# Optimization experiments

Hardware: AMD Instinct MI355X
Metric: run time of the kernel (lower is better)

## Reference

```python
import jax, jax.numpy as jnp
import numpy as np

B, N, IN_DIM, OUT_DIM, H = 4, 2048, 1024, 1024, 16
HEAD_DIM = OUT_DIM // H  # 64


def setup_inputs() -> dict:
    key = jax.random.key(0)
    k_x, k_q, k_k, k_v, k_o = jax.random.split(key, 5)
    s = 1.0 / np.sqrt(IN_DIM)
    return {
        "x": jax.random.normal(k_x, (B, N, IN_DIM), dtype=jnp.float32),
        "w_q": jax.random.normal(k_q, (IN_DIM, OUT_DIM), dtype=jnp.float32) * s,
        "w_k": jax.random.normal(k_k, (IN_DIM, OUT_DIM), dtype=jnp.float32) * s,
        "w_v": jax.random.normal(k_v, (IN_DIM, OUT_DIM), dtype=jnp.float32) * s,
        "w_out": jax.random.normal(k_o, (OUT_DIM, OUT_DIM), dtype=jnp.float32) * s,
    }


def reference(x, w_q, w_k, w_v, w_out):
    b, n, _ = x.shape
    scale = 1.0 / jnp.sqrt(jnp.float32(HEAD_DIM))
    # QKV projections, split into heads: [b, h, n, d]
    q = (x @ w_q).reshape(b, n, H, HEAD_DIM).transpose(0, 2, 1, 3)
    k = (x @ w_k).reshape(b, n, H, HEAD_DIM).transpose(0, 2, 1, 3)
    v = (x @ w_v).reshape(b, n, H, HEAD_DIM).transpose(0, 2, 1, 3)
    # full score matrix [b, h, q, k]
    scores = jnp.einsum("bhqd,bhkd->bhqk", q, k) * scale
    # NOTE: source applies softmax over dim=1 (the HEAD axis) — reproduce exactly
    attn = jax.nn.softmax(scores, axis=1)
    # dropout p=0.0 -> identity
    ctx = jnp.einsum("bhqk,bhkd->bqhd", attn, v).reshape(b, n, OUT_DIM)
    return ctx @ w_out
```

## Files before the change

kernel.cpp:

```cpp
#include <hip/hip_runtime.h>
#include <hip/hip_bf16.h>

typedef unsigned short u16;
typedef unsigned int u32;
typedef __attribute__((ext_vector_type(8))) short short8;
typedef __attribute__((ext_vector_type(4))) float float4v;
typedef __attribute__((ext_vector_type(4))) unsigned int uint4v;
typedef __attribute__((ext_vector_type(2))) unsigned int uint2v;

__device__ __forceinline__ u16 f2bf(float f) {
    union { float f; unsigned int u; } v; v.f = f;
    unsigned int r = v.u + 0x7fffu + ((v.u >> 16) & 1u);
    return (u16)(r >> 16);
}

__device__ __forceinline__ u32 cvtpk(float lo, float hi) {
    u32 r;
    asm("v_cvt_pk_bf16_f32 %0, %1, %2" : "=v"(r) : "v"(lo), "v"(hi));
    return r;
}
__device__ __forceinline__ float bflo(u32 u) {
    union { u32 u; float f; } v; v.u = u << 16; return v.f;
}
__device__ __forceinline__ float bfhi(u32 u) {
    union { u32 u; float f; } v; v.u = u & 0xffff0000u; return v.f;
}

__device__ __forceinline__ void gld_lds16(const u16* g, u16* l) {
    __builtin_amdgcn_global_load_lds(
        (const __attribute__((address_space(1))) u32*)g,
        (__attribute__((address_space(3))) u32*)l, 16, 0, 0);
}

__global__ __launch_bounds__(256) void convert_x(
    const float* __restrict__ x, u16* __restrict__ xb) {
    int i = (blockIdx.x * 256 + threadIdx.x) * 8;
    float4v a = *(const float4v*)&x[i];
    float4v b = *(const float4v*)&x[i + 4];
    u16 tmp[8] __attribute__((aligned(16)));
#pragma unroll
    for (int j = 0; j < 4; ++j) { tmp[j] = f2bf(a[j]); tmp[4 + j] = f2bf(b[j]); }
    *(uint4v*)&xb[i] = *(uint4v*)tmp;
}

__global__ __launch_bounds__(256) void transpose_w(
    const float* __restrict__ w0, const float* __restrict__ w1,
    const float* __restrict__ w2, const float* __restrict__ w3,
    u16* __restrict__ o0, u16* __restrict__ o1,
    u16* __restrict__ o2, u16* __restrict__ o3) {
    __shared__ u16 t[32][33];
    int z = blockIdx.z;
    const float* w = (z == 0) ? w0 : (z == 1) ? w1 : (z == 2) ? w2 : w3;
    u16* o         = (z == 0) ? o0 : (z == 1) ? o1 : (z == 2) ? o2 : o3;
    int bx = blockIdx.x * 32;
    int by = blockIdx.y * 32;
    int x = threadIdx.x, y = threadIdx.y;
#pragma unroll
    for (int i = 0; i < 4; ++i)
        t[y + i * 8][x] = f2bf(w[(size_t)(by + y + i * 8) * 1024 + bx + x]);
    __syncthreads();
#pragma unroll
    for (int i = 0; i < 4; ++i)
        o[(size_t)(bx + y + i * 8) * 1024 + by + x] = t[x][y + i * 8];
}

__global__ __launch_bounds__(256) void gemm_bt(
    const u16* __restrict__ A, const u16* __restrict__ Bt,
    void* __restrict__ Cout, int M, int N, int K, int mode, float oscale) {
    __shared__ __attribute__((aligned(16))) u16 As[128 * 32];
    __shared__ __attribute__((aligned(16))) u16 Bs[128 * 32];
    const int tid = threadIdx.x;
    const int m0 = blockIdx.y * 128;
    const int n0 = blockIdx.x * 128;
    const int wid = tid >> 6;
    const int lane = tid & 63;
    const int ln = lane & 15, kq = lane >> 4;
    const int wm = (wid >> 1) * 64, wn = (wid & 1) * 64;

    float4v acc[4][4] = {};
    for (int k0 = 0; k0 < K; k0 += 32) {
#pragma unroll
        for (int i = 0; i < 2; ++i) {
            int chunk = tid + i * 256;
            int row = chunk >> 2, cg = chunk & 3;
            u16* lA = &As[(size_t)(i * 256 + wid * 64) * 8];
            u16* lB = &Bs[(size_t)(i * 256 + wid * 64) * 8];
            gld_lds16(&A[(size_t)(m0 + row) * K + k0 + cg * 8], lA);
            gld_lds16(&Bt[(size_t)(n0 + row) * K + k0 + cg * 8], lB);
        }
        __syncthreads();
        short8 af[4], bfr[4];
#pragma unroll
        for (int mt = 0; mt < 4; ++mt)
            af[mt] = *(const short8*)&As[(wm + mt * 16 + ln) * 32 + kq * 8];
#pragma unroll
        for (int nt = 0; nt < 4; ++nt)
            bfr[nt] = *(const short8*)&Bs[(wn + nt * 16 + ln) * 32 + kq * 8];
#pragma unroll
        for (int mt = 0; mt < 4; ++mt)
#pragma unroll
            for (int nt = 0; nt < 4; ++nt)
                acc[mt][nt] = __builtin_amdgcn_mfma_f32_16x16x32_bf16(
                    af[mt], bfr[nt], acc[mt][nt], 0, 0, 0);
        __syncthreads();
    }
    if (mode == 0) {
        u16* C = (u16*)Cout;
#pragma unroll
        for (int mt = 0; mt < 4; ++mt)
#pragma unroll
            for (int nt = 0; nt < 4; ++nt)
#pragma unroll
                for (int r = 0; r < 4; ++r) {
                    int row = m0 + wm + mt * 16 + kq * 4 + r;
                    int col = n0 + wn + nt * 16 + ln;
                    C[(size_t)row * N + col] = f2bf(acc[mt][nt][r] * oscale);
                }
    } else if (mode == 1) {
        u16* C = (u16*)Cout;
#pragma unroll
        for (int mt = 0; mt < 4; ++mt)
#pragma unroll
            for (int nt = 0; nt < 4; ++nt)
#pragma unroll
                for (int r = 0; r < 4; ++r) {
                    int t = m0 + wm + mt * 16 + kq * 4 + r;
                    int col = n0 + wn + nt * 16 + ln;
                    int b = t >> 11, n = t & 2047;
                    C[((size_t)(b * 1024 + col)) * 2048 + n] = f2bf(acc[mt][nt][r]);
                }
    } else {
        float* C = (float*)Cout;
#pragma unroll
        for (int mt = 0; mt < 4; ++mt)
#pragma unroll
            for (int nt = 0; nt < 4; ++nt)
#pragma unroll
                for (int r = 0; r < 4; ++r) {
                    int row = m0 + wm + mt * 16 + kq * 4 + r;
                    int col = n0 + wn + nt * 16 + ln;
                    C[(size_t)row * N + col] = acc[mt][nt][r];
                }
    }
}

__global__ __launch_bounds__(1024, 4) void attn_kernel(
    const u16* qb, const u16* __restrict__ kb,
    const u16* __restrict__ vt, u16* cb) {
    __shared__ __attribute__((aligned(16))) u16   Ebuf[3][512 * 36];
    __shared__ __attribute__((aligned(16))) float Dibuf[2][32 * 36];

    const int b = blockIdx.y;
    const int q0 = blockIdx.x * 32;
    const int tid = threadIdx.x;
    const int wid = tid >> 6, lane = tid & 63;
    const int ln = lane & 15, kq = lane >> 4;
    const int h = wid;

    short8 aq[2][2];
#pragma unroll
    for (int mt = 0; mt < 2; ++mt)
#pragma unroll
        for (int kc = 0; kc < 2; ++kc)
            aq[mt][kc] = *(const short8*)&qb[
                (size_t)(b * 2048 + q0 + mt * 16 + ln) * 1024 +
                h * 64 + kc * 32 + kq * 8];

    float4v cacc[2][4] = {};
    short8 bvA[4], bvB[4];

    const int NT = 64;
#pragma unroll 1
    for (int i = 0; i < NT + 2; ++i) {
        short8 bk[2][2];
        if (i < NT) {
            const int kt = i * 32;
#pragma unroll
            for (int kc = 0; kc < 2; ++kc)
#pragma unroll
                for (int nt = 0; nt < 2; ++nt)
                    bk[kc][nt] = *(const short8*)&kb[
                        (size_t)(b * 2048 + kt + nt * 16 + ln) * 1024 +
                        h * 64 + kc * 32 + kq * 8];
        }
        if (i >= 1 && i <= NT) {
            const int kt = (i - 1) * 32;
#pragma unroll
            for (int nt = 0; nt < 4; ++nt)
                bvB[nt] = *(const short8*)&vt[
                    (size_t)(b * 1024 + h * 64 + nt * 16 + ln) * 2048 + kt + kq * 8];
        }
        if (i >= 2) {
            const u16*   Ee = Ebuf[(i - 2) % 3];
            const float* Dd = Dibuf[(i - 2) & 1];
            short8 ap[2];
#pragma unroll
            for (int mt = 0; mt < 2; ++mt) {
                const u16* ep = &Ee[(h * 32 + mt * 16 + ln) * 36 + kq * 8];
                uint2v ea = *(const uint2v*)&ep[0];
                uint2v eb = *(const uint2v*)&ep[4];
                const float* dp = &Dd[(mt * 16 + ln) * 36 + kq * 8];
                float4v g0 = *(const float4v*)&dp[0];
                float4v g1 = *(const float4v*)&dp[4];
                u32 pk[4] __attribute__((aligned(16)));
                pk[0] = cvtpk(bflo(ea[0]) * g0[0], bfhi(ea[0]) * g0[1]);
                pk[1] = cvtpk(bflo(ea[1]) * g0[2], bfhi(ea[1]) * g0[3]);
                pk[2] = cvtpk(bflo(eb[0]) * g1[0], bfhi(eb[0]) * g1[1]);
                pk[3] = cvtpk(bflo(eb[1]) * g1[2], bfhi(eb[1]) * g1[3]);
                ap[mt] = *(short8*)pk;
            }
#pragma unroll
            for (int nt = 0; nt < 4; ++nt)
#pragma unroll
                for (int mt = 0; mt < 2; ++mt)
                    cacc[mt][nt] = __builtin_amdgcn_mfma_f32_16x16x32_bf16(
                        ap[mt], bvA[nt], cacc[mt][nt], 0, 0, 0);
        }
        if (i < NT) {
            float4v sacc[2][2] = {};
#pragma unroll
            for (int kc = 0; kc < 2; ++kc)
#pragma unroll
                for (int mt = 0; mt < 2; ++mt)
#pragma unroll
                    for (int nt = 0; nt < 2; ++nt)
                        sacc[mt][nt] = __builtin_amdgcn_mfma_f32_16x16x32_bf16(
                            bk[kc][nt], aq[mt][kc], sacc[mt][nt], 0, 0, 0);
            u16* Ew = Ebuf[i % 3];
#pragma unroll
            for (int mt = 0; mt < 2; ++mt)
#pragma unroll
                for (int nt = 0; nt < 2; ++nt) {
                    float e0 = exp2f(fminf(sacc[mt][nt][0], 115.0f));
                    float e1 = exp2f(fminf(sacc[mt][nt][1], 115.0f));
                    float e2 = exp2f(fminf(sacc[mt][nt][2], 115.0f));
                    float e3 = exp2f(fminf(sacc[mt][nt][3], 115.0f));
                    uint2v w; w[0] = cvtpk(e0, e1); w[1] = cvtpk(e2, e3);
                    *(uint2v*)&Ew[(h * 32 + mt * 16 + ln) * 36 + nt * 16 + kq * 4] = w;
                }
        }
        if (i >= 1 && i <= NT && tid < 256) {
            const u16* Ee = Ebuf[(i - 1) % 3];
            const int q = tid >> 3, k4 = tid & 7;
            float d0 = 0.f, d1 = 0.f, d2 = 0.f, d3 = 0.f;
#pragma unroll
            for (int hh = 0; hh < 16; ++hh) {
                uint2v e = *(const uint2v*)&Ee[(hh * 32 + q) * 36 + k4 * 4];
                d0 += bflo(e[0]); d1 += bfhi(e[0]);
                d2 += bflo(e[1]); d3 += bfhi(e[1]);
            }
            float4v dv;
            dv[0] = __builtin_amdgcn_rcpf(d0);
            dv[1] = __builtin_amdgcn_rcpf(d1);
            dv[2] = __builtin_amdgcn_rcpf(d2);
            dv[3] = __builtin_amdgcn_rcpf(d3);
            *(float4v*)&Dibuf[(i - 1) & 1][q * 36 + k4 * 4] = dv;
        }
        __syncthreads();
#pragma unroll
        for (int nt = 0; nt < 4; ++nt) bvA[nt] = bvB[nt];
    }

#pragma unroll
    for (int mt = 0; mt < 2; ++mt)
#pragma unroll
        for (int nt = 0; nt < 4; ++nt)
#pragma unroll
            for (int r = 0; r < 4; ++r) {
                int row = b * 2048 + q0 + mt * 16 + kq * 4 + r;
                int col = h * 64 + nt * 16 + ln;
                cb[(size_t)row * 1024 + col] = f2bf(cacc[mt][nt][r]);
            }
}

extern "C" void kernel_launch(void* const* d_in, const int* in_sizes, int n_in,
                              void* d_out, int out_size, void* d_ws, size_t ws_size,
                              hipStream_t stream) {
    const float* x   = (const float*)d_in[0];
    const float* w_q = (const float*)d_in[1];
    const float* w_k = (const float*)d_in[2];
    const float* w_v = (const float*)d_in[3];
    const float* w_o = (const float*)d_in[4];

    char* ws = (char*)d_ws;
    const size_t SZ_W   = (size_t)1024 * 1024 * 2;
    const size_t SZ_TOK = (size_t)8192 * 1024 * 2;
    u16* x_bf  = (u16*)(ws);
    u16* wtq   = (u16*)(ws + SZ_TOK);
    u16* wtk   = (u16*)(ws + SZ_TOK + SZ_W);
    u16* wtv   = (u16*)(ws + SZ_TOK + 2 * SZ_W);
    u16* wto   = (u16*)(ws + SZ_TOK + 3 * SZ_W);
    u16* q_buf = (u16*)(ws + SZ_TOK + 4 * SZ_W);
    u16* k_buf  = (u16*)d_out;
    u16* vt_buf = (u16*)d_out + (size_t)8192 * 1024;

    convert_x<<<4096, 256, 0, stream>>>(x, x_bf);

    transpose_w<<<dim3(32, 32, 4), dim3(32, 8), 0, stream>>>(
        w_q, w_k, w_v, w_o, wtq, wtk, wtv, wto);

    gemm_bt<<<dim3(8, 64), 256, 0, stream>>>(x_bf, wtq, q_buf, 8192, 1024, 1024, 0, 0.18033688f);
    gemm_bt<<<dim3(8, 64), 256, 0, stream>>>(x_bf, wtk, k_buf, 8192, 1024, 1024, 0, 1.0f);
    gemm_bt<<<dim3(8, 64), 256, 0, stream>>>(x_bf, wtv, vt_buf, 8192, 1024, 1024, 1, 1.0f);

    attn_kernel<<<dim3(64, 4), 1024, 0, stream>>>(q_buf, k_buf, vt_buf, q_buf);

    gemm_bt<<<dim3(8, 64), 256, 0, stream>>>(q_buf, wto, d_out, 8192, 1024, 1024, 2, 1.0f);
}
```

Measured before the change: 536.5 us.

## Replace three-stage attention pipeline with 64-key tiles and two barriers per tile

```diff
diff --git a/kernel.cpp b/kernel.cpp
--- a/kernel.cpp
+++ b/kernel.cpp
@@ -7,6 +7,7 @@
 typedef __attribute__((ext_vector_type(4))) float float4v;
 typedef __attribute__((ext_vector_type(4))) unsigned int uint4v;
 typedef __attribute__((ext_vector_type(2))) unsigned int uint2v;
+typedef __attribute__((ext_vector_type(2))) float float2v;
 
 __device__ __forceinline__ u16 f2bf(float f) {
     union { float f; unsigned int u; } v; v.f = f;
@@ -144,11 +145,11 @@
     }
 }
 
-__global__ __launch_bounds__(1024, 4) void attn_kernel(
+__global__ __launch_bounds__(1024) void attn_kernel(
     const u16* qb, const u16* __restrict__ kb,
     const u16* __restrict__ vt, u16* cb) {
-    __shared__ __attribute__((aligned(16))) u16   Ebuf[3][512 * 36];
-    __shared__ __attribute__((aligned(16))) float Dibuf[2][32 * 36];
+    __shared__ __attribute__((aligned(16))) u16   Ebuf[2][512 * 72];
+    __shared__ __attribute__((aligned(16))) float Di[32 * 68];
 
     const int b = blockIdx.y;
     const int q0 = blockIdx.x * 32;
@@ -167,39 +168,83 @@
                 h * 64 + kc * 32 + kq * 8];
 
     float4v cacc[2][4] = {};
-    short8 bvA[4], bvB[4];
-
-    const int NT = 64;
+
 #pragma unroll 1
-    for (int i = 0; i < NT + 2; ++i) {
-        short8 bk[2][2];
-        if (i < NT) {
-            const int kt = i * 32;
+    for (int t = 0; t < 32; ++t) {
+        const int kt = t << 6;
+        u16* E = Ebuf[t & 1];
+
+#pragma unroll
+        for (int c = 0; c < 2; ++c) {
+            short8 bk[2][2];
 #pragma unroll
             for (int kc = 0; kc < 2; ++kc)
 #pragma unroll
                 for (int nt = 0; nt < 2; ++nt)
                     bk[kc][nt] = *(const short8*)&kb[
-                        (size_t)(b * 2048 + kt + nt * 16 + ln) * 1024 +
+                        (size_t)(b * 2048 + kt + c * 32 + nt * 16 + ln) * 1024 +
                         h * 64 + kc * 32 + kq * 8];
+            float4v sacc[2][2] = {};
+#pragma unroll
+            for (int kc = 0; kc < 2; ++kc)
+#pragma unroll
+                for (int mt = 0; mt < 2; ++mt)
+#pragma unroll
+                    for (int nt = 0; nt < 2; ++nt)
+                        sacc[mt][nt] = __builtin_amdgcn_mfma_f32_16x16x32_bf16(
+                            bk[kc][nt], aq[mt][kc], sacc[mt][nt], 0, 0, 0);
+#pragma unroll
+            for (int mt = 0; mt < 2; ++mt)
+#pragma unroll
+                for (int nt = 0; nt < 2; ++nt) {
+                    float e0 = exp2f(fminf(sacc[mt][nt][0], 115.0f));
+                    float e1 = exp2f(fminf(sacc[mt][nt][1], 115.0f));
+                    float e2 = exp2f(fminf(sacc[mt][nt][2], 115.0f));
+                    float e3 = exp2f(fminf(sacc[mt][nt][3], 115.0f));
+                    uint2v w; w[0] = cvtpk(e0, e1); w[1] = cvtpk(e2, e3);
+                    *(uint2v*)&E[(h * 32 + mt * 16 + ln) * 72 +
+                                 c * 32 + nt * 16 + kq * 4] = w;
+                }
         }
-        if (i >= 1 && i <= NT) {
-            const int kt = (i - 1) * 32;
-#pragma unroll
-            for (int nt = 0; nt < 4; ++nt)
-                bvB[nt] = *(const short8*)&vt[
-                    (size_t)(b * 1024 + h * 64 + nt * 16 + ln) * 2048 + kt + kq * 8];
+
+        short8 bv[2][4];
+#pragma unroll
+        for (int c = 0; c < 2; ++c)
+#pragma unroll
+            for (int nt = 0; nt < 4; ++nt)
+                bv[c][nt] = *(const short8*)&vt[
+                    (size_t)(b * 1024 + h * 64 + nt * 16 + ln) * 2048 +
+                    kt + c * 32 + kq * 8];
+
+        __syncthreads();
+
+        {
+            const int q = tid >> 5, kk = tid & 31;
+            const u16* ec = &E[q * 72 + 2 * kk];
+            float d0 = 0.f, d1 = 0.f, d2 = 0.f, d3 = 0.f;
+#pragma unroll
+            for (int hh = 0; hh < 8; ++hh) {
+                u32 ea = *(const u32*)&ec[(2 * hh) * (32 * 72)];
+                u32 eb = *(const u32*)&ec[(2 * hh + 1) * (32 * 72)];
+                d0 += bflo(ea); d1 += bfhi(ea);
+                d2 += bflo(eb); d3 += bfhi(eb);
+            }
+            float2v dv;
+            dv[0] = __builtin_amdgcn_rcpf(d0 + d2);
+            dv[1] = __builtin_amdgcn_rcpf(d1 + d3);
+            *(float2v*)&Di[q * 68 + 2 * kk] = dv;
         }
-        if (i >= 2) {
-            const u16*   Ee = Ebuf[(i - 2) % 3];
-            const float* Dd = Dibuf[(i - 2) & 1];
+        __syncthreads();
+
+#pragma unroll
+        for (int mt = 0; mt < 2; ++mt) {
             short8 ap[2];
 #pragma unroll
-            for (int mt = 0; mt < 2; ++mt) {
-                const u16* ep = &Ee[(h * 32 + mt * 16 + ln) * 36 + kq * 8];
+            for (int c = 0; c < 2; ++c) {
+                const u16* ep = &E[(h * 32 + mt * 16 + ln) * 72 + c * 32 + kq * 8];
                 uint2v ea = *(const uint2v*)&ep[0];
                 uint2v eb = *(const uint2v*)&ep[4];
-                const float* dp = &Dd[(mt * 16 + ln) * 36 + kq * 8];
+                const float* dp = &Di[(mt * 16 + ln) * 68 + c * 32 + kq * 8];
                 float4v g0 = *(const float4v*)&dp[0];
                 float4v g1 = *(const float4v*)&dp[4];
                 u32 pk[4] __attribute__((aligned(16)));
@@ -207,58 +252,16 @@
                 pk[1] = cvtpk(bflo(ea[1]) * g0[2], bfhi(ea[1]) * g0[3]);
                 pk[2] = cvtpk(bflo(eb[0]) * g1[0], bfhi(eb[0]) * g1[1]);
                 pk[3] = cvtpk(bflo(eb[1]) * g1[2], bfhi(eb[1]) * g1[3]);
-                ap[mt] = *(short8*)pk;
+                ap[c] = *(short8*)pk;
             }
 #pragma unroll
-            for (int nt = 0; nt < 4; ++nt)
-#pragma unroll
-                for (int mt = 0; mt < 2; ++mt)
-                    cacc[mt][nt] = __builtin_amdgcn_mfma_f32_16x16x32_bf16(
-                        ap[mt], bvA[nt], cacc[mt][nt], 0, 0, 0);
+            for (int nt = 0; nt < 4; ++nt) {
+                cacc[mt][nt] = __builtin_amdgcn_mfma_f32_16x16x32_bf16(
+                    ap[0], bv[0][nt], cacc[mt][nt], 0, 0, 0);
+                cacc[mt][nt] = __builtin_amdgcn_mfma_f32_16x16x32_bf16(
+                    ap[1], bv[1][nt], cacc[mt][nt], 0, 0, 0);
+            }
         }
-        if (i < NT) {
-            float4v sacc[2][2] = {};
-#pragma unroll
-            for (int kc = 0; kc < 2; ++kc)
-#pragma unroll
-                for (int mt = 0; mt < 2; ++mt)
-#pragma unroll
-                    for (int nt = 0; nt < 2; ++nt)
-                        sacc[mt][nt] = __builtin_amdgcn_mfma_f32_16x16x32_bf16(
-                            bk[kc][nt], aq[mt][kc], sacc[mt][nt], 0, 0, 0);
-            u16* Ew = Ebuf[i % 3];
-#pragma unroll
-            for (int mt = 0; mt < 2; ++mt)
-#pragma unroll
-                for (int nt = 0; nt < 2; ++nt) {
-                    float e0 = exp2f(fminf(sacc[mt][nt][0], 115.0f));
-                    float e1 = exp2f(fminf(sacc[mt][nt][1], 115.0f));
-                    float e2 = exp2f(fminf(sacc[mt][nt][2], 115.0f));
-                    float e3 = exp2f(fminf(sacc[mt][nt][3], 115.0f));
-                    uint2v w; w[0] = cvtpk(e0, e1); w[1] = cvtpk(e2, e3);
-                    *(uint2v*)&Ew[(h * 32 + mt * 16 + ln) * 36 + nt * 16 + kq * 4] = w;
-                }
-        }
-        if (i >= 1 && i <= NT && tid < 256) {
-            const u16* Ee = Ebuf[(i - 1) % 3];
-            const int q = tid >> 3, k4 = tid & 7;
-            float d0 = 0.f, d1 = 0.f, d2 = 0.f, d3 = 0.f;
-#pragma unroll
-            for (int hh = 0; hh < 16; ++hh) {
-                uint2v e = *(const uint2v*)&Ee[(hh * 32 + q) * 36 + k4 * 4];
-                d0 += bflo(e[0]); d1 += bfhi(e[0]);
-                d2 += bflo(e[1]); d3 += bfhi(e[1]);
-            }
-            float4v dv;
-            dv[0] = __builtin_amdgcn_rcpf(d0);
-            dv[1] = __builtin_amdgcn_rcpf(d1);
-            dv[2] = __builtin_amdgcn_rcpf(d2);
-            dv[3] = __builtin_amdgcn_rcpf(d3);
-            *(float4v*)&Dibuf[(i - 1) & 1][q * 36 + k4 * 4] = dv;
-        }
-        __syncthreads();
-#pragma unroll
-        for (int nt = 0; nt < 4; ++nt) bvA[nt] = bvB[nt];
     }
 
 #pragma unroll
```

Result: faster. 482.5 us (-10.1%).
